# Kernel tuning notes

Hardware: AMD Instinct MI355X
Metric: run time of the kernel (lower is better)

The kernel has to match this reference:

```python
import jax, jax.numpy as jnp
import numpy as np

N_NODES = 100000
N_EDGES = 1600000
IN_DIM = 128
HID_DIM = 128
OUT_DIM = 64
NUM_GRAPHS = 64


def setup_inputs() -> dict:
    key = jax.random.key(0)
    k = jax.random.split(key, 8)
    x = jax.random.normal(k[0], (N_NODES, IN_DIM), dtype=jnp.float32)
    edge_index = jax.random.randint(k[1], (2, N_EDGES), 0, N_NODES, dtype=jnp.int64)
    batch = jnp.sort(jax.random.randint(k[2], (N_NODES,), 0, NUM_GRAPHS, dtype=jnp.int64))
    # glorot-ish init for GCN weights, zero bias (PyG default)
    W1 = jax.random.normal(k[3], (IN_DIM, HID_DIM), dtype=jnp.float32) / np.sqrt(IN_DIM)
    b1 = jnp.zeros((HID_DIM,), dtype=jnp.float32)
    W2 = jax.random.normal(k[4], (HID_DIM, OUT_DIM), dtype=jnp.float32) / np.sqrt(HID_DIM)
    b2 = jnp.zeros((OUT_DIM,), dtype=jnp.float32)
    return {"x": x, "edge_index": edge_index, "batch": batch,
            "W1": W1, "b1": b1, "W2": W2, "b2": b2}


def _gcn_conv(x, W, b, src, dst, norm, n_nodes):
    # x' = scatter_add_{dst}(norm * (xW)[src]) + b   (self-loops already in src/dst)
    h = x @ W                              # [N, D_out]
    msg = norm[:, None] * h[src]           # [E+N, D_out] gather + scale
    out = jax.ops.segment_sum(msg, dst, num_segments=n_nodes)
    return out + b


def _gcn_norm(src, dst, n_nodes):
    # symmetric normalization with self-loops: deg^-1/2[src] * deg^-1/2[dst]
    deg = jax.ops.segment_sum(jnp.ones_like(dst, dtype=jnp.float32), dst,
                              num_segments=n_nodes)
    dinv = jnp.where(deg > 0, jax.lax.rsqrt(deg), 0.0)
    return dinv[src] * dinv[dst]


def reference(x, edge_index, batch, W1, b1, W2, b2):
    n = x.shape[0]
    loops = jnp.arange(n, dtype=edge_index.dtype)
    src = jnp.concatenate([edge_index[0], loops])
    dst = jnp.concatenate([edge_index[1], loops])
    norm = _gcn_norm(src, dst, n)

    h = jax.nn.relu(_gcn_conv(x, W1, b1, src, dst, norm, n))
    h = jax.nn.relu(_gcn_conv(h, W2, b2, src, dst, norm, n))

    # global mean pool per graph
    sums = jax.ops.segment_sum(h, batch, num_segments=NUM_GRAPHS)
    cnts = jax.ops.segment_sum(jnp.ones((n,), dtype=h.dtype), batch,
                               num_segments=NUM_GRAPHS)
    return sums / jnp.maximum(cnts, 1.0)[:, None]
```

## Files before the change

kernel.cpp:

```cpp
#include <hip/hip_runtime.h>

typedef unsigned short ushort_t;
typedef unsigned int uint_t;
typedef __attribute__((ext_vector_type(8))) short bf16x8;
typedef __attribute__((ext_vector_type(4))) float f32x4;

__device__ inline ushort_t bf16_rne(float f) {
    uint_t u = __float_as_uint(f);
    return (ushort_t)((u + 0x7FFFu + ((u >> 16) & 1u)) >> 16);
}

__device__ inline float4 bf4_to_f4(uint2 v) {
    float4 f;
    f.x = __uint_as_float(v.x << 16);
    f.y = __uint_as_float(v.x & 0xFFFF0000u);
    f.z = __uint_as_float(v.y << 16);
    f.w = __uint_as_float(v.y & 0xFFFF0000u);
    return f;
}


#define BSH 8
#define NBMAX 512
#define EPB 4096

__global__ __launch_bounds__(256) void k_bhist(const int* __restrict__ dst,
                                               int* __restrict__ bcnt, int E, int nb) {
    __shared__ int h[NBMAX];
    const int tid = threadIdx.x;
    for (int i = tid; i < NBMAX; i += 256) h[i] = 0;
    __syncthreads();
    const int e0 = blockIdx.x * EPB;
    for (int i = tid; i < EPB; i += 256) {
        int e = e0 + i;
        if (e < E) atomicAdd(&h[dst[e] >> BSH], 1);
    }
    __syncthreads();
    for (int i = tid; i < nb; i += 256)
        if (h[i]) atomicAdd(&bcnt[i], h[i]);
}

__global__ __launch_bounds__(512) void k_bscan(const int* __restrict__ bcnt,
                                               int* __restrict__ boff,
                                               int* __restrict__ bcur, int nb) {
    __shared__ int a[NBMAX];
    const int t = threadIdx.x;
    int v = (t < nb) ? bcnt[t] : 0;
    a[t] = v;
    __syncthreads();
    for (int off = 1; off < NBMAX; off <<= 1) {
        int x = (t >= off) ? a[t - off] : 0;
        __syncthreads();
        a[t] += x;
        __syncthreads();
    }
    if (t < nb) {
        int excl = a[t] - v;
        boff[t] = excl;
        bcur[t] = excl;
    }
}

__global__ __launch_bounds__(256) void k_bscatter(const int* __restrict__ src,
                                                  const int* __restrict__ dst,
                                                  int* __restrict__ bcur,
                                                  int2* __restrict__ pairs, int E, int nb) {
    __shared__ int h[NBMAX];
    __shared__ int base[NBMAX];
    const int tid = threadIdx.x;
    for (int i = tid; i < NBMAX; i += 256) h[i] = 0;
    __syncthreads();
    const int e0 = blockIdx.x * EPB;
    for (int i = tid; i < EPB; i += 256) {
        int e = e0 + i;
        if (e < E) atomicAdd(&h[dst[e] >> BSH], 1);
    }
    __syncthreads();
    for (int b = tid; b < nb; b += 256) {
        int c = h[b];
        base[b] = c ? atomicAdd(&bcur[b], c) : 0;
        h[b] = 0;
    }
    __syncthreads();
    for (int i = tid; i < EPB; i += 256) {
        int e = e0 + i;
        if (e < E) {
            int s = src[e], d = dst[e];
            int bk = d >> BSH;
            int off = atomicAdd(&h[bk], 1);
            pairs[base[bk] + off] = make_int2(s, d);
        }
    }
}

__global__ __launch_bounds__(256) void k_bcsr(const int2* __restrict__ pairs,
                                              const int* __restrict__ boff,
                                              const int* __restrict__ bcurEnd,
                                              int* __restrict__ rowptr,
                                              int* __restrict__ rowend,
                                              float* __restrict__ dinv,
                                              int* __restrict__ csr, int n) {
    __shared__ int deg[256], sc[256], cur[256];
    const int t = threadIdx.x;
    const int b = blockIdx.x;
    const int beg = boff[b], end = bcurEnd[b];
    deg[t] = 0;
    __syncthreads();
    for (int i = beg + t; i < end; i += 256) {
        int2 p = pairs[i];
        atomicAdd(&deg[p.y & 255], 1);
    }
    __syncthreads();
    int dv = deg[t];
    sc[t] = dv;
    __syncthreads();
    for (int off = 1; off < 256; off <<= 1) {
        int x = (t >= off) ? sc[t - off] : 0;
        __syncthreads();
        sc[t] += x;
        __syncthreads();
    }
    int excl = sc[t] - dv;
    cur[t] = excl;
    int d = (b << BSH) + t;
    if (d < n) {
        int r = beg + excl;
        rowptr[d] = r;
        rowend[d] = r + dv;
        dinv[d] = rsqrtf((float)dv + 1.0f);
    }
    __syncthreads();
    for (int i = beg + t; i < end; i += 256) {
        int2 p = pairs[i];
        int off = atomicAdd(&cur[p.y & 255], 1);
        csr[beg + off] = p.x;
    }
}


__global__ __launch_bounds__(256) void k_prep_w(const float* __restrict__ W1,
                                                const float* __restrict__ W2,
                                                ushort_t* __restrict__ Wt1,
                                                ushort_t* __restrict__ Wt2) {
    int idx = blockIdx.x * 256 + threadIdx.x;
    if (idx < 16384) {
        int k = idx >> 7, c = idx & 127;
        Wt1[c * 128 + k] = bf16_rne(W1[idx]);
    } else if (idx < 24576) {
        int j = idx - 16384;
        int k = j >> 6, c = j & 63;
        Wt2[c * 128 + k] = bf16_rne(W2[j]);
    }
}


template <int DOUT, bool IN_BF16>
__global__ __launch_bounds__(256) void k_gemm_mfma(const void* __restrict__ Xv,
                                                   const ushort_t* __restrict__ Wt,
                                                   const float* __restrict__ dinv,
                                                   ushort_t* __restrict__ G, int n) {
    constexpr int KP = 136;
    constexpr int NW = DOUT / 2;
    constexpr int NT = NW / 16;
    __shared__ ushort_t Xs[128 * KP];
    __shared__ ushort_t Ws[DOUT * KP];

    const int tid = threadIdx.x;
    const int row0 = blockIdx.x * 128;

    if (!IN_BF16) {
        const float* X = (const float*)Xv;
#pragma unroll
        for (int i = 0; i < 16; i++) {
            int idx = tid * 4 + i * 1024;
            int r = idx >> 7, k = idx & 127;
            int gr = row0 + r;
            float4 v = make_float4(0.f, 0.f, 0.f, 0.f);
            if (gr < n) v = *(const float4*)&X[(size_t)gr * 128 + k];
            ushort4 o;
            o.x = bf16_rne(v.x); o.y = bf16_rne(v.y);
            o.z = bf16_rne(v.z); o.w = bf16_rne(v.w);
            *(ushort4*)&Xs[r * KP + k] = o;
        }
    } else {
        const ushort_t* X = (const ushort_t*)Xv;
#pragma unroll
        for (int i = 0; i < 8; i++) {
            int idx = tid * 8 + i * 2048;
            int r = idx >> 7, k = idx & 127;
            int gr = row0 + r;
            uint4 v = make_uint4(0u, 0u, 0u, 0u);
            if (gr < n) v = *(const uint4*)&X[(size_t)gr * 128 + k];
            *(uint4*)&Xs[r * KP + k] = v;
        }
    }
    constexpr int WI = (DOUT * 128) / 2048;
#pragma unroll
    for (int i = 0; i < WI; i++) {
        int idx = tid * 8 + i * 2048;
        int r = idx >> 7, k = idx & 127;
        *(uint4*)&Ws[r * KP + k] = *(const uint4*)&Wt[idx];
    }
    __syncthreads();

    const int lane = tid & 63;
    const int wid = tid >> 6;
    const int wm = wid & 1, wn = wid >> 1;
    const int lr = lane & 15;
    const int kg = lane >> 4;

    f32x4 acc[4][NT];
#pragma unroll
    for (int mi = 0; mi < 4; mi++)
#pragma unroll
        for (int ni = 0; ni < NT; ni++)
#pragma unroll
            for (int q = 0; q < 4; q++) acc[mi][ni][q] = 0.f;

    const ushort_t* xb = &Xs[(wm * 64 + lr) * KP + kg * 8];
    const ushort_t* wb = &Ws[(wn * NW + lr) * KP + kg * 8];

#pragma unroll
    for (int ks = 0; ks < 4; ks++) {
        bf16x8 a[4], b[NT];
#pragma unroll
        for (int mi = 0; mi < 4; mi++)
            a[mi] = *(const bf16x8*)&xb[mi * 16 * KP + ks * 32];
#pragma unroll
        for (int ni = 0; ni < NT; ni++)
            b[ni] = *(const bf16x8*)&wb[ni * 16 * KP + ks * 32];
#pragma unroll
        for (int mi = 0; mi < 4; mi++)
#pragma unroll
            for (int ni = 0; ni < NT; ni++)
                acc[mi][ni] = __builtin_amdgcn_mfma_f32_16x16x32_bf16(
                    a[mi], b[ni], acc[mi][ni], 0, 0, 0);
    }

#pragma unroll
    for (int mi = 0; mi < 4; mi++) {
        int r0 = row0 + wm * 64 + mi * 16 + kg * 4;
#pragma unroll
        for (int r = 0; r < 4; r++) {
            int gr = r0 + r;
            if (gr < n) {
                float s = dinv[gr];
#pragma unroll
                for (int ni = 0; ni < NT; ni++) {
                    int c = wn * NW + ni * 16 + lr;
                    G[(size_t)gr * DOUT + c] = bf16_rne(s * acc[mi][ni][r]);
                }
            }
        }
    }
}


__global__ __launch_bounds__(256) void k_gather128(const int* __restrict__ rowptr,
                                                   const int* __restrict__ rowend,
                                                   const int* __restrict__ csr,
                                                   const ushort_t* __restrict__ G,
                                                   const float* __restrict__ dinv,
                                                   const float* __restrict__ b,
                                                   ushort_t* __restrict__ H, int n) {
    const int g = blockIdx.x * 8 + threadIdx.x / 32;
    const int lane = threadIdx.x & 31;
    if (g >= n) return;
    const int beg = rowptr[g], end = rowend[g];

    float4 acc = bf4_to_f4(*(const uint2*)&G[(size_t)g * 128 + lane * 4]);
    int e = beg;
    for (; e + 3 < end; e += 4) {
        int s0 = csr[e], s1 = csr[e + 1], s2 = csr[e + 2], s3 = csr[e + 3];
        uint2 r0 = *(const uint2*)&G[(size_t)s0 * 128 + lane * 4];
        uint2 r1 = *(const uint2*)&G[(size_t)s1 * 128 + lane * 4];
        uint2 r2 = *(const uint2*)&G[(size_t)s2 * 128 + lane * 4];
        uint2 r3 = *(const uint2*)&G[(size_t)s3 * 128 + lane * 4];
        float4 a0 = bf4_to_f4(r0), a1 = bf4_to_f4(r1);
        float4 a2 = bf4_to_f4(r2), a3 = bf4_to_f4(r3);
        acc.x += (a0.x + a1.x) + (a2.x + a3.x);
        acc.y += (a0.y + a1.y) + (a2.y + a3.y);
        acc.z += (a0.z + a1.z) + (a2.z + a3.z);
        acc.w += (a0.w + a1.w) + (a2.w + a3.w);
    }
    for (; e < end; e++) {
        int s0 = csr[e];
        float4 a = bf4_to_f4(*(const uint2*)&G[(size_t)s0 * 128 + lane * 4]);
        acc.x += a.x; acc.y += a.y; acc.z += a.z; acc.w += a.w;
    }
    const float di = dinv[g];
    float4 bb = *(const float4*)&b[lane * 4];
    ushort4 o;
    o.x = bf16_rne(fmaxf(di * acc.x + bb.x, 0.f));
    o.y = bf16_rne(fmaxf(di * acc.y + bb.y, 0.f));
    o.z = bf16_rne(fmaxf(di * acc.z + bb.z, 0.f));
    o.w = bf16_rne(fmaxf(di * acc.w + bb.w, 0.f));
    *(ushort4*)&H[(size_t)g * 128 + lane * 4] = o;
}


__global__ __launch_bounds__(256) void k_gather64_pool(const int* __restrict__ rowptr,
                                                       const int* __restrict__ rowend,
                                                       const int* __restrict__ csr,
                                                       const ushort_t* __restrict__ G,
                                                       const float* __restrict__ dinv,
                                                       const float* __restrict__ b,
                                                       const int* __restrict__ batch,
                                                       float* __restrict__ pool, int n) {
    __shared__ float po[16][68];
    __shared__ int pg[16];
    const int grp = threadIdx.x / 16;
    const int lane = threadIdx.x & 15;
    const int g = blockIdx.x * 16 + grp;

    float4 o = make_float4(0.f, 0.f, 0.f, 0.f);
    if (g < n) {
        const int beg = rowptr[g], end = rowend[g];
        float4 acc = bf4_to_f4(*(const uint2*)&G[(size_t)g * 64 + lane * 4]);
        int e = beg;
        for (; e + 3 < end; e += 4) {
            int s0 = csr[e], s1 = csr[e + 1], s2 = csr[e + 2], s3 = csr[e + 3];
            uint2 r0 = *(const uint2*)&G[(size_t)s0 * 64 + lane * 4];
            uint2 r1 = *(const uint2*)&G[(size_t)s1 * 64 + lane * 4];
            uint2 r2 = *(const uint2*)&G[(size_t)s2 * 64 + lane * 4];
            uint2 r3 = *(const uint2*)&G[(size_t)s3 * 64 + lane * 4];
            float4 a0 = bf4_to_f4(r0), a1 = bf4_to_f4(r1);
            float4 a2 = bf4_to_f4(r2), a3 = bf4_to_f4(r3);
            acc.x += (a0.x + a1.x) + (a2.x + a3.x);
            acc.y += (a0.y + a1.y) + (a2.y + a3.y);
            acc.z += (a0.z + a1.z) + (a2.z + a3.z);
            acc.w += (a0.w + a1.w) + (a2.w + a3.w);
        }
        for (; e < end; e++) {
            int s0 = csr[e];
            float4 a = bf4_to_f4(*(const uint2*)&G[(size_t)s0 * 64 + lane * 4]);
            acc.x += a.x; acc.y += a.y; acc.z += a.z; acc.w += a.w;
        }
        const float di = dinv[g];
        float4 bb = *(const float4*)&b[lane * 4];
        o.x = fmaxf(di * acc.x + bb.x, 0.f);
        o.y = fmaxf(di * acc.y + bb.y, 0.f);
        o.z = fmaxf(di * acc.z + bb.z, 0.f);
        o.w = fmaxf(di * acc.w + bb.w, 0.f);
    }
    if (lane == 0) pg[grp] = (g < n) ? batch[g] : -1;
    *(float4*)&po[grp][lane * 4] = o;
    __syncthreads();

    if (threadIdx.x < 64) {
        const int c = threadIdx.x;
        float run = 0.f;
        int cur = -1;
        for (int r = 0; r < 16; r++) {
            int gr = pg[r];
            if (gr < 0) continue;
            if (gr != cur) {
                if (cur >= 0) atomicAdd(&pool[cur * 64 + c], run);
                cur = gr;
                run = 0.f;
            }
            run += po[r][c];
        }
        if (cur >= 0) atomicAdd(&pool[cur * 64 + c], run);
    }
}


__global__ __launch_bounds__(64) void k_div_bs(const float* __restrict__ pool,
                                               const int* __restrict__ batch,
                                               float* __restrict__ out, int n) {
    int t = blockIdx.x * 64 + threadIdx.x;
    int g = t >> 6;
    int lo = 0, hi = n;
    while (lo < hi) { int m = (lo + hi) >> 1; if (batch[m] < g) lo = m + 1; else hi = m; }
    int lb = lo;
    lo = lb; hi = n;
    while (lo < hi) { int m = (lo + hi) >> 1; if (batch[m] <= g) lo = m + 1; else hi = m; }
    float c = (float)(lo - lb);
    c = c > 1.f ? c : 1.f;
    out[t] = pool[t] / c;
}


extern "C" void kernel_launch(void* const* d_in, const int* in_sizes, int n_in,
                              void* d_out, int out_size, void* d_ws, size_t ws_size,
                              hipStream_t stream) {
    const float* x = (const float*)d_in[0];
    const int* edge = (const int*)d_in[1];
    const int* batch = (const int*)d_in[2];
    const float* W1 = (const float*)d_in[3];
    const float* b1 = (const float*)d_in[4];
    const float* W2 = (const float*)d_in[5];
    const float* b2 = (const float*)d_in[6];

    const int n = in_sizes[0] / 128;
    const int E = in_sizes[1] / 2;
    const int* src = edge;
    const int* dst = edge + E;
    const int nb = (n + 255) >> BSH;

    size_t nA = ((size_t)n + 255) & ~(size_t)255;
    float* dinv = (float*)d_ws;
    int* rowptr = (int*)(dinv + nA);
    int* rowend = rowptr + nA;
    int* bcnt = rowend + nA;
    int* boff = bcnt + NBMAX;
    int* bcur = boff + NBMAX;
    float* pool = (float*)(bcur + NBMAX);
    ushort_t* Wt1 = (ushort_t*)(pool + 4096 + 256);
    ushort_t* Wt2 = Wt1 + 16384;
    ushort_t* bufG = Wt2 + 8192;
    ushort_t* bufH = bufG + (size_t)n * 128;
    int* csr = (int*)(bufH + (size_t)n * 128);
    int2* pairs = (int2*)bufG;

    hipMemsetAsync(bcnt, 0, NBMAX * 4, stream);
    hipMemsetAsync(pool, 0, 4096 * 4, stream);

    k_prep_w<<<96, 256, 0, stream>>>(W1, W2, Wt1, Wt2);

    int gE = (E + EPB - 1) / EPB;
    k_bhist<<<gE, 256, 0, stream>>>(dst, bcnt, E, nb);
    k_bscan<<<1, NBMAX, 0, stream>>>(bcnt, boff, bcur, nb);
    k_bscatter<<<gE, 256, 0, stream>>>(src, dst, bcur, pairs, E, nb);
    k_bcsr<<<nb, 256, 0, stream>>>(pairs, boff, bcur, rowptr, rowend, dinv, csr, n);

    k_gemm_mfma<128, false><<<(n + 127) / 128, 256, 0, stream>>>(x, Wt1, dinv, bufG, n);
    k_gather128<<<(n + 7) / 8, 256, 0, stream>>>(rowptr, rowend, csr, bufG, dinv, b1,
                                                 bufH, n);

    k_gemm_mfma<64, true><<<(n + 127) / 128, 256, 0, stream>>>(bufH, Wt2, dinv, bufG, n);
    k_gather64_pool<<<(n + 15) / 16, 256, 0, stream>>>(rowptr, rowend, csr, bufG, dinv,
                                                       b2, batch, pool, n);

    k_div_bs<<<64, 64, 0, stream>>>(pool, batch, (float*)d_out, n);
}
```

Measured before the change: 228.3 us.

## Fuse layer-1 aggregation into layer-2 GEMM and widen gather loads

Merges the layer-1 neighbor gather (bias, ReLU, bf16 pack) with the layer-2 MFMA GEMM. Each block aggregates 128 rows straight into shared memory and multiplies them by W2, so the intermediate H buffer is never written to or reread from global memory. Both gather kernels now load 16-byte vectors of 8 bf16 per lane instead of 8-byte loads, with fewer lanes per row. The pool kernel handles 32 rows per block. The trade-off is that the fused kernel has only 782 blocks with 16 rows in flight per iteration, which may reduce latency hiding for the irregular gathers.

```diff
diff --git a/kernel.cpp b/kernel.cpp
--- a/kernel.cpp
+++ b/kernel.cpp
@@ -10,13 +10,30 @@
     return (ushort_t)((u + 0x7FFFu + ((u >> 16) & 1u)) >> 16);
 }
 
-__device__ inline float4 bf4_to_f4(uint2 v) {
-    float4 f;
-    f.x = __uint_as_float(v.x << 16);
-    f.y = __uint_as_float(v.x & 0xFFFF0000u);
-    f.z = __uint_as_float(v.y << 16);
-    f.w = __uint_as_float(v.y & 0xFFFF0000u);
-    return f;
+__device__ inline uint_t pack2(float lo, float hi) {
+    return (uint_t)bf16_rne(lo) | ((uint_t)bf16_rne(hi) << 16);
+}
+
+__device__ inline void acc8(uint4 v, float* a) {
+    a[0] += __uint_as_float(v.x << 16);
+    a[1] += __uint_as_float(v.x & 0xFFFF0000u);
+    a[2] += __uint_as_float(v.y << 16);
+    a[3] += __uint_as_float(v.y & 0xFFFF0000u);
+    a[4] += __uint_as_float(v.z << 16);
+    a[5] += __uint_as_float(v.z & 0xFFFF0000u);
+    a[6] += __uint_as_float(v.w << 16);
+    a[7] += __uint_as_float(v.w & 0xFFFF0000u);
+}
+
+__device__ inline void set8(uint4 v, float* a) {
+    a[0] = __uint_as_float(v.x << 16);
+    a[1] = __uint_as_float(v.x & 0xFFFF0000u);
+    a[2] = __uint_as_float(v.y << 16);
+    a[3] = __uint_as_float(v.y & 0xFFFF0000u);
+    a[4] = __uint_as_float(v.z << 16);
+    a[5] = __uint_as_float(v.z & 0xFFFF0000u);
+    a[6] = __uint_as_float(v.w << 16);
+    a[7] = __uint_as_float(v.w & 0xFFFF0000u);
 }
 
 
@@ -154,49 +171,32 @@
 }
 
 
-template <int DOUT, bool IN_BF16>
-__global__ __launch_bounds__(256) void k_gemm_mfma(const void* __restrict__ Xv,
-                                                   const ushort_t* __restrict__ Wt,
-                                                   const float* __restrict__ dinv,
-                                                   ushort_t* __restrict__ G, int n) {
+__global__ __launch_bounds__(256) void k_gemm1(const float* __restrict__ X,
+                                               const ushort_t* __restrict__ Wt,
+                                               const float* __restrict__ dinv,
+                                               ushort_t* __restrict__ G, int n) {
     constexpr int KP = 136;
-    constexpr int NW = DOUT / 2;
-    constexpr int NT = NW / 16;
+    constexpr int NW = 64, NT = 4;
     __shared__ ushort_t Xs[128 * KP];
-    __shared__ ushort_t Ws[DOUT * KP];
+    __shared__ ushort_t Ws[128 * KP];
 
     const int tid = threadIdx.x;
     const int row0 = blockIdx.x * 128;
 
-    if (!IN_BF16) {
-        const float* X = (const float*)Xv;
-#pragma unroll
-        for (int i = 0; i < 16; i++) {
-            int idx = tid * 4 + i * 1024;
-            int r = idx >> 7, k = idx & 127;
-            int gr = row0 + r;
-            float4 v = make_float4(0.f, 0.f, 0.f, 0.f);
-            if (gr < n) v = *(const float4*)&X[(size_t)gr * 128 + k];
-            ushort4 o;
-            o.x = bf16_rne(v.x); o.y = bf16_rne(v.y);
-            o.z = bf16_rne(v.z); o.w = bf16_rne(v.w);
-            *(ushort4*)&Xs[r * KP + k] = o;
-        }
-    } else {
-        const ushort_t* X = (const ushort_t*)Xv;
-#pragma unroll
-        for (int i = 0; i < 8; i++) {
-            int idx = tid * 8 + i * 2048;
-            int r = idx >> 7, k = idx & 127;
-            int gr = row0 + r;
-            uint4 v = make_uint4(0u, 0u, 0u, 0u);
-            if (gr < n) v = *(const uint4*)&X[(size_t)gr * 128 + k];
-            *(uint4*)&Xs[r * KP + k] = v;
-        }
-    }
-    constexpr int WI = (DOUT * 128) / 2048;
-#pragma unroll
-    for (int i = 0; i < WI; i++) {
+#pragma unroll
+    for (int i = 0; i < 16; i++) {
+        int idx = tid * 4 + i * 1024;
+        int r = idx >> 7, k = idx & 127;
+        int gr = row0 + r;
+        float4 v = make_float4(0.f, 0.f, 0.f, 0.f);
+        if (gr < n) v = *(const float4*)&X[(size_t)gr * 128 + k];
+        ushort4 o;
+        o.x = bf16_rne(v.x); o.y = bf16_rne(v.y);
+        o.z = bf16_rne(v.z); o.w = bf16_rne(v.w);
+        *(ushort4*)&Xs[r * KP + k] = o;
+    }
+#pragma unroll
+    for (int i = 0; i < 8; i++) {
         int idx = tid * 8 + i * 2048;
         int r = idx >> 7, k = idx & 127;
         *(uint4*)&Ws[r * KP + k] = *(const uint4*)&Wt[idx];
@@ -206,8 +206,7 @@
     const int lane = tid & 63;
     const int wid = tid >> 6;
     const int wm = wid & 1, wn = wid >> 1;
-    const int lr = lane & 15;
-    const int kg = lane >> 4;
+    const int lr = lane & 15, kg = lane >> 4;
 
     f32x4 acc[4][NT];
 #pragma unroll
@@ -248,7 +247,7 @@
 #pragma unroll
                 for (int ni = 0; ni < NT; ni++) {
                     int c = wn * NW + ni * 16 + lr;
-                    G[(size_t)gr * DOUT + c] = bf16_rne(s * acc[mi][ni][r]);
+                    G[(size_t)gr * 128 + c] = bf16_rne(s * acc[mi][ni][r]);
                 }
             }
         }
@@ -256,46 +255,113 @@
 }
 
 
-__global__ __launch_bounds__(256) void k_gather128(const int* __restrict__ rowptr,
-                                                   const int* __restrict__ rowend,
-                                                   const int* __restrict__ csr,
-                                                   const ushort_t* __restrict__ G,
-                                                   const float* __restrict__ dinv,
-                                                   const float* __restrict__ b,
-                                                   ushort_t* __restrict__ H, int n) {
-    const int g = blockIdx.x * 8 + threadIdx.x / 32;
-    const int lane = threadIdx.x & 31;
-    if (g >= n) return;
-    const int beg = rowptr[g], end = rowend[g];
-
-    float4 acc = bf4_to_f4(*(const uint2*)&G[(size_t)g * 128 + lane * 4]);
-    int e = beg;
-    for (; e + 3 < end; e += 4) {
-        int s0 = csr[e], s1 = csr[e + 1], s2 = csr[e + 2], s3 = csr[e + 3];
-        uint2 r0 = *(const uint2*)&G[(size_t)s0 * 128 + lane * 4];
-        uint2 r1 = *(const uint2*)&G[(size_t)s1 * 128 + lane * 4];
-        uint2 r2 = *(const uint2*)&G[(size_t)s2 * 128 + lane * 4];
-        uint2 r3 = *(const uint2*)&G[(size_t)s3 * 128 + lane * 4];
-        float4 a0 = bf4_to_f4(r0), a1 = bf4_to_f4(r1);
-        float4 a2 = bf4_to_f4(r2), a3 = bf4_to_f4(r3);
-        acc.x += (a0.x + a1.x) + (a2.x + a3.x);
-        acc.y += (a0.y + a1.y) + (a2.y + a3.y);
-        acc.z += (a0.z + a1.z) + (a2.z + a3.z);
-        acc.w += (a0.w + a1.w) + (a2.w + a3.w);
-    }
-    for (; e < end; e++) {
-        int s0 = csr[e];
-        float4 a = bf4_to_f4(*(const uint2*)&G[(size_t)s0 * 128 + lane * 4]);
-        acc.x += a.x; acc.y += a.y; acc.z += a.z; acc.w += a.w;
-    }
-    const float di = dinv[g];
-    float4 bb = *(const float4*)&b[lane * 4];
-    ushort4 o;
-    o.x = bf16_rne(fmaxf(di * acc.x + bb.x, 0.f));
-    o.y = bf16_rne(fmaxf(di * acc.y + bb.y, 0.f));
-    o.z = bf16_rne(fmaxf(di * acc.z + bb.z, 0.f));
-    o.w = bf16_rne(fmaxf(di * acc.w + bb.w, 0.f));
-    *(ushort4*)&H[(size_t)g * 128 + lane * 4] = o;
+__global__ __launch_bounds__(256) void k_gather_gemm2(const int* __restrict__ rowptr,
+                                                      const int* __restrict__ rowend,
+                                                      const int* __restrict__ csr,
+                                                      const ushort_t* __restrict__ G1,
+                                                      const float* __restrict__ dinv,
+                                                      const float* __restrict__ b1,
+                                                      const ushort_t* __restrict__ Wt2,
+                                                      ushort_t* __restrict__ G2, int n) {
+    constexpr int KP = 136;
+    __shared__ ushort_t Xs[128 * KP];
+    __shared__ ushort_t Ws[64 * KP];
+
+    const int tid = threadIdx.x;
+    const int row0 = blockIdx.x * 128;
+
+#pragma unroll
+    for (int i = 0; i < 4; i++) {
+        int idx = tid * 8 + i * 2048;
+        int r = idx >> 7, k = idx & 127;
+        *(uint4*)&Ws[r * KP + k] = *(const uint4*)&Wt2[idx];
+    }
+
+    const int grp = tid >> 4;
+    const int lane = tid & 15;
+    const int koff = lane * 8;
+    for (int it = 0; it < 8; it++) {
+        int r = grp + it * 16;
+        int g = row0 + r;
+        uint4 ov = make_uint4(0u, 0u, 0u, 0u);
+        if (g < n) {
+            float a[8];
+            set8(*(const uint4*)&G1[(size_t)g * 128 + koff], a);
+            int e = rowptr[g];
+            const int end = rowend[g];
+            for (; e + 3 < end; e += 4) {
+                int s0 = csr[e], s1 = csr[e + 1], s2 = csr[e + 2], s3 = csr[e + 3];
+                uint4 v0 = *(const uint4*)&G1[(size_t)s0 * 128 + koff];
+                uint4 v1 = *(const uint4*)&G1[(size_t)s1 * 128 + koff];
+                uint4 v2 = *(const uint4*)&G1[(size_t)s2 * 128 + koff];
+                uint4 v3 = *(const uint4*)&G1[(size_t)s3 * 128 + koff];
+                acc8(v0, a); acc8(v1, a); acc8(v2, a); acc8(v3, a);
+            }
+            for (; e < end; e++) {
+                int s0 = csr[e];
+                acc8(*(const uint4*)&G1[(size_t)s0 * 128 + koff], a);
+            }
+            const float di = dinv[g];
+            float4 bb0 = *(const float4*)&b1[koff];
+            float4 bb1 = *(const float4*)&b1[koff + 4];
+            ov.x = pack2(fmaxf(di * a[0] + bb0.x, 0.f), fmaxf(di * a[1] + bb0.y, 0.f));
+            ov.y = pack2(fmaxf(di * a[2] + bb0.z, 0.f), fmaxf(di * a[3] + bb0.w, 0.f));
+            ov.z = pack2(fmaxf(di * a[4] + bb1.x, 0.f), fmaxf(di * a[5] + bb1.y, 0.f));
+            ov.w = pack2(fmaxf(di * a[6] + bb1.z, 0.f), fmaxf(di * a[7] + bb1.w, 0.f));
+        }
+        *(uint4*)&Xs[r * KP + koff] = ov;
+    }
+    __syncthreads();
+
+    const int lane64 = tid & 63;
+    const int wid = tid >> 6;
+    const int wm = wid & 1, wn = wid >> 1;
+    const int lr = lane64 & 15, kg = lane64 >> 4;
+
+    f32x4 acc[4][2];
+#pragma unroll
+    for (int mi = 0; mi < 4; mi++)
+#pragma unroll
+        for (int ni = 0; ni < 2; ni++)
+#pragma unroll
+            for (int q = 0; q < 4; q++) acc[mi][ni][q] = 0.f;
+
+    const ushort_t* xb = &Xs[(wm * 64 + lr) * KP + kg * 8];
+    const ushort_t* wb = &Ws[(wn * 32 + lr) * KP + kg * 8];
+
+#pragma unroll
+    for (int ks = 0; ks < 4; ks++) {
+        bf16x8 a[4], b[2];
+#pragma unroll
+        for (int mi = 0; mi < 4; mi++)
+            a[mi] = *(const bf16x8*)&xb[mi * 16 * KP + ks * 32];
+#pragma unroll
+        for (int ni = 0; ni < 2; ni++)
+            b[ni] = *(const bf16x8*)&wb[ni * 16 * KP + ks * 32];
+#pragma unroll
+        for (int mi = 0; mi < 4; mi++)
+#pragma unroll
+            for (int ni = 0; ni < 2; ni++)
+                acc[mi][ni] = __builtin_amdgcn_mfma_f32_16x16x32_bf16(
+                    a[mi], b[ni], acc[mi][ni], 0, 0, 0);
+    }
+
+#pragma unroll
+    for (int mi = 0; mi < 4; mi++) {
+        int r0 = row0 + wm * 64 + mi * 16 + kg * 4;
+#pragma unroll
+        for (int r = 0; r < 4; r++) {
+            int gr = r0 + r;
+            if (gr < n) {
+                float s = dinv[gr];
+#pragma unroll
+                for (int ni = 0; ni < 2; ni++) {
+                    int c = wn * 32 + ni * 16 + lr;
+                    G2[(size_t)gr * 64 + c] = bf16_rne(s * acc[mi][ni][r]);
+                }
+            }
+        }
+    }
 }
 
 
@@ -307,51 +373,53 @@
                                                        const float* __restrict__ b,
                                                        const int* __restrict__ batch,
                                                        float* __restrict__ pool, int n) {
-    __shared__ float po[16][68];
-    __shared__ int pg[16];
-    const int grp = threadIdx.x / 16;
-    const int lane = threadIdx.x & 15;
-    const int g = blockIdx.x * 16 + grp;
-
-    float4 o = make_float4(0.f, 0.f, 0.f, 0.f);
+    __shared__ float po[32][72];
+    __shared__ int pg[32];
+    const int grp = threadIdx.x >> 3;
+    const int lane = threadIdx.x & 7;
+    const int g = blockIdx.x * 32 + grp;
+    const int koff = lane * 8;
+
+    float o8[8] = {0.f, 0.f, 0.f, 0.f, 0.f, 0.f, 0.f, 0.f};
     if (g < n) {
-        const int beg = rowptr[g], end = rowend[g];
-        float4 acc = bf4_to_f4(*(const uint2*)&G[(size_t)g * 64 + lane * 4]);
-        int e = beg;
+        float a[8];
+        set8(*(const uint4*)&G[(size_t)g * 64 + koff], a);
+        int e = rowptr[g];
+        const int end = rowend[g];
         for (; e + 3 < end; e += 4) {
             int s0 = csr[e], s1 = csr[e + 1], s2 = csr[e + 2], s3 = csr[e + 3];
-            uint2 r0 = *(const uint2*)&G[(size_t)s0 * 64 + lane * 4];
-            uint2 r1 = *(const uint2*)&G[(size_t)s1 * 64 + lane * 4];
-            uint2 r2 = *(const uint2*)&G[(size_t)s2 * 64 + lane * 4];
-            uint2 r3 = *(const uint2*)&G[(size_t)s3 * 64 + lane * 4];
-            float4 a0 = bf4_to_f4(r0), a1 = bf4_to_f4(r1);
-            float4 a2 = bf4_to_f4(r2), a3 = bf4_to_f4(r3);
-            acc.x += (a0.x + a1.x) + (a2.x + a3.x);
-            acc.y += (a0.y + a1.y) + (a2.y + a3.y);
-            acc.z += (a0.z + a1.z) + (a2.z + a3.z);
-            acc.w += (a0.w + a1.w) + (a2.w + a3.w);
+            uint4 v0 = *(const uint4*)&G[(size_t)s0 * 64 + koff];
+            uint4 v1 = *(const uint4*)&G[(size_t)s1 * 64 + koff];
+            uint4 v2 = *(const uint4*)&G[(size_t)s2 * 64 + koff];
+            uint4 v3 = *(const uint4*)&G[(size_t)s3 * 64 + koff];
+            acc8(v0, a); acc8(v1, a); acc8(v2, a); acc8(v3, a);
         }
         for (; e < end; e++) {
             int s0 = csr[e];
-            float4 a = bf4_to_f4(*(const uint2*)&G[(size_t)s0 * 64 + lane * 4]);
-            acc.x += a.x; acc.y += a.y; acc.z += a.z; acc.w += a.w;
+            acc8(*(const uint4*)&G[(size_t)s0 * 64 + koff], a);
         }
         const float di = dinv[g];
-        float4 bb = *(const float4*)&b[lane * 4];
-        o.x = fmaxf(di * acc.x + bb.x, 0.f);
-        o.y = fmaxf(di * acc.y + bb.y, 0.f);
-        o.z = fmaxf(di * acc.z + bb.z, 0.f);
-        o.w = fmaxf(di * acc.w + bb.w, 0.f);
+        float4 bb0 = *(const float4*)&b[koff];
+        float4 bb1 = *(const float4*)&b[koff + 4];
+        o8[0] = fmaxf(di * a[0] + bb0.x, 0.f);
+        o8[1] = fmaxf(di * a[1] + bb0.y, 0.f);
+        o8[2] = fmaxf(di * a[2] + bb0.z, 0.f);
+        o8[3] = fmaxf(di * a[3] + bb0.w, 0.f);
+        o8[4] = fmaxf(di * a[4] + bb1.x, 0.f);
+        o8[5] = fmaxf(di * a[5] + bb1.y, 0.f);
+        o8[6] = fmaxf(di * a[6] + bb1.z, 0.f);
+        o8[7] = fmaxf(di * a[7] + bb1.w, 0.f);
     }
     if (lane == 0) pg[grp] = (g < n) ? batch[g] : -1;
-    *(float4*)&po[grp][lane * 4] = o;
+    *(float4*)&po[grp][koff] = make_float4(o8[0], o8[1], o8[2], o8[3]);
+    *(float4*)&po[grp][koff + 4] = make_float4(o8[4], o8[5], o8[6], o8[7]);
     __syncthreads();
 
     if (threadIdx.x < 64) {
         const int c = threadIdx.x;
         float run = 0.f;
         int cur = -1;
-        for (int r = 0; r < 16; r++) {
+        for (int r = 0; r < 32; r++) {
             int gr = pg[r];
             if (gr < 0) continue;
             if (gr != cur) {
@@ -409,10 +477,10 @@
     float* pool = (float*)(bcur + NBMAX);
     ushort_t* Wt1 = (ushort_t*)(pool + 4096 + 256);
     ushort_t* Wt2 = Wt1 + 16384;
-    ushort_t* bufG = Wt2 + 8192;
-    ushort_t* bufH = bufG + (size_t)n * 128;
-    int* csr = (int*)(bufH + (size_t)n * 128);
-    int2* pairs = (int2*)bufG;
+    ushort_t* bufG1 = Wt2 + 8192;
+    ushort_t* bufG2 = bufG1 + (size_t)n * 128;
+    int* csr = (int*)(bufG2 + (size_t)n * 64);
+    int2* pairs = (int2*)bufG1;
 
     hipMemsetAsync(bcnt, 0, NBMAX * 4, stream);
     hipMemsetAsync(pool, 0, 4096 * 4, stream);
@@ -425,13 +493,13 @@
     k_bscatter<<<gE, 256, 0, stream>>>(src, dst, bcur, pairs, E, nb);
     k_bcsr<<<nb, 256, 0, stream>>>(pairs, boff, bcur, rowptr, rowend, dinv, csr, n);
 
-    k_gemm_mfma<128, false><<<(n + 127) / 128, 256, 0, stream>>>(x, Wt1, dinv, bufG, n);
-    k_gather128<<<(n + 7) / 8, 256, 0, stream>>>(rowptr, rowend, csr, bufG, dinv, b1,
-                                                 bufH, n);
-
-    k_gemm_mfma<64, true><<<(n + 127) / 128, 256, 0, stream>>>(bufH, Wt2, dinv, bufG, n);
-    k_gather64_pool<<<(n + 15) / 16, 256, 0, stream>>>(rowptr, rowend, csr, bufG, dinv,
-                                                       b2, batch, pool, n);
+    k_gemm1<<<(n + 127) / 128, 256, 0, stream>>>(x, Wt1, dinv, bufG1, n);
+
+    k_gather_gemm2<<<(n + 127) / 128, 256, 0, stream>>>(rowptr, rowend, csr, bufG1,
+                                                        dinv, b1, Wt2, bufG2, n);
+
+    k_gather64_pool<<<(n + 31) / 32, 256, 0, stream>>>(rowptr, rowend, csr, bufG2,
+                                                       dinv, b2, batch, pool, n);
 
     k_div_bs<<<64, 64, 0, stream>>>(pool, batch, (float*)d_out, n);
 }
```

Result: slower. 243.2 us (+6.5%).
